# Performance work log

Hardware: AMD Instinct MI355X
Metric: run time of the kernel (lower is better)

Reference implementation:

```python
import jax, jax.numpy as jnp
import numpy as np

NUM_HEADS = 12
HEAD_DIM = 64
NPT = 1  # num_prefix_tokens

def _rot(x):
    # pairs (x0,x1) -> (-x1, x0), matching timm's rot()
    x2 = x.reshape(*x.shape[:-1], -1, 2)
    r = jnp.stack([-x2[..., 1], x2[..., 0]], axis=-1)
    return r.reshape(x.shape)

def _apply_rope_cat(x, rope):
    # rope: [N_rot, 2*hd] = sin||cos concatenated
    sin, cos = jnp.split(rope, 2, axis=-1)
    return x * cos + _rot(x) * sin

def setup_inputs() -> dict:
    key = jax.random.key(0)
    ks = jax.random.split(key, 7)
    B, N, C = 8, 4097, 768
    hd = HEAD_DIM
    x = jax.random.normal(ks[0], (B, N, C), jnp.float32)
    rope = jax.random.normal(ks[1], (N - NPT, 2 * hd), jnp.float32)
    qkv_w = jax.random.normal(ks[2], (3 * C, C), jnp.float32) * (C ** -0.5)
    q_bias = jax.random.normal(ks[3], (C,), jnp.float32) * 0.02
    v_bias = jax.random.normal(ks[4], (C,), jnp.float32) * 0.02
    proj_w = jax.random.normal(ks[5], (C, C), jnp.float32) * (C ** -0.5)
    proj_b = jax.random.normal(ks[6], (C,), jnp.float32) * 0.02
    return dict(x=x, rope=rope, qkv_w=qkv_w, q_bias=q_bias, v_bias=v_bias,
                proj_w=proj_w, proj_b=proj_b)

def reference(x, rope, qkv_w, q_bias, v_bias, proj_w, proj_b):
    B, N, C = x.shape
    H, hd = NUM_HEADS, HEAD_DIM
    # fused QKV with k_bias fixed at zero (non-trainable buffer)
    bias = jnp.concatenate([q_bias, jnp.zeros_like(q_bias), v_bias])
    qkv = x @ qkv_w.T + bias                            # [B,N,3C]
    qkv = qkv.reshape(B, N, 3, H, hd).transpose(2, 0, 3, 1, 4)
    q, k, v = qkv[0], qkv[1], qkv[2]                    # [B,H,N,hd]
    # RoPE on all tokens except the prefix (CLS) token
    q = jnp.concatenate([q[:, :, :NPT], _apply_rope_cat(q[:, :, NPT:], rope)], axis=2)
    k = jnp.concatenate([k[:, :, :NPT], _apply_rope_cat(k[:, :, NPT:], rope)], axis=2)
    # linear attention: kv = K^T V, then Q @ kv, normalized by hd*N
    kv = jnp.einsum('bhnd,bhne->bhde', k, v)            # [B,H,hd,hd]
    out = jnp.einsum('bhnd,bhde->bhne', q, kv) / hd / N # [B,H,N,hd]
    out = out.transpose(0, 2, 1, 3).reshape(B, N, C)
    return out @ proj_w.T + proj_b
```

## Files before the change

### kernel.cpp

```cpp
#include <hip/hip_runtime.h>
#include <hip/hip_bf16.h>

typedef __attribute__((ext_vector_type(8))) short short8;
typedef __attribute__((ext_vector_type(4))) float f32x4;

#define B_    8
#define N_    4097
#define C_    768
#define M_TOT (B_*N_)
#define K3    (3*C_)
#define CHUNKS 16
#define NSTEP 24

__device__ __forceinline__ float bf2f(unsigned short u) {
  union { unsigned int i; float f; } x; x.i = ((unsigned int)u) << 16; return x.f;
}
__device__ __forceinline__ unsigned short f2bf(float f) {
  union { float f; unsigned int i; } x; x.f = f;
  unsigned int i = x.i + 0x7fffu + ((x.i >> 16) & 1u);
  return (unsigned short)(i >> 16);
}
__device__ __forceinline__ void gload16(const void* g, void* l) {
  __builtin_amdgcn_global_load_lds(
      (const __attribute__((address_space(1))) void*)g,
      (__attribute__((address_space(3))) void*)l, 16, 0, 0);
}

__global__ __launch_bounds__(256) void cvt_kernel(const float* __restrict__ inx,
                                                  unsigned short* __restrict__ outx,
                                                  const float* __restrict__ inw,
                                                  unsigned short* __restrict__ outw,
                                                  long n4x, long n4tot) {
  long i = (long)blockIdx.x * blockDim.x + threadIdx.x;
  long stride = (long)gridDim.x * blockDim.x;
  for (; i < n4tot; i += stride) {
    const float4* src; ushort4* dst; long j;
    if (i < n4x) { src = (const float4*)inx; dst = (ushort4*)outx; j = i; }
    else         { src = (const float4*)inw; dst = (ushort4*)outw; j = i - n4x; }
    float4 v = src[j];
    ushort4 o;
    o.x = f2bf(v.x); o.y = f2bf(v.y); o.z = f2bf(v.z); o.w = f2bf(v.w);
    dst[j] = o;
  }
}

__global__ __launch_bounds__(512, 4) void gemm_qkv_rope(
    const unsigned short* __restrict__ A,
    const unsigned short* __restrict__ Bw,
    const float* __restrict__ rope,
    const float* __restrict__ qb,
    const float* __restrict__ vb,
    unsigned short* __restrict__ qkv)
{
  __shared__ __align__(16) char L[3*24576];
  const int tid  = threadIdx.x;
  const int wave = tid >> 6, lane = tid & 63;
  const int lr = lane & 15, lk = lane >> 4;
  const int wm = wave >> 2, wn = wave & 3;

  const int o = blockIdx.x;
  const int xcd = o & 7, loc = o >> 3;
  const int tile = (xcd < 1 ? xcd*290 : 290 + (xcd-1)*289) + loc;
  const int m0 = (tile / 9) * 128;
  const int n0 = (tile % 9) * 256;

  const int arow = tid >> 2, achk = tid & 3;
  const int am = min(m0 + arow, M_TOT-1);
  const unsigned short* gA  = A  + (long)am*768 + achk*8;
  const unsigned short* gB1 = Bw + (long)(n0 + arow)*768 + achk*8;
  const unsigned short* gB2 = Bw + (long)(n0 + arow + 128)*768 + achk*8;
  const int dA  = wave*1024;
  const int dB1 = 8192  + wave*1024;
  const int dB2 = 16384 + wave*1024;

  const int abase = (wm*64 + lr)*64 + lk*16;
  const int bbase = 8192 + (wn*64 + lr)*64 + lk*16;

  f32x4 acc[4][4];
#pragma unroll
  for (int i = 0; i < 4; ++i)
#pragma unroll
    for (int j = 0; j < 4; ++j) acc[i][j] = (f32x4){0.f,0.f,0.f,0.f};

  auto STAGE = [&](int buf, int kk) {
    char* sb = L + buf*24576;
    gload16(gA  + kk, sb + dA);
    gload16(gB1 + kk, sb + dB1);
    gload16(gB2 + kk, sb + dB2);
  };
  auto COMPUTE = [&](int buf) {
    const char* sb = L + buf*24576;
    short8 af[4], bfr[4];
#pragma unroll
    for (int mi = 0; mi < 4; ++mi)
      af[mi] = *(const short8*)(sb + abase + mi*1024);
#pragma unroll
    for (int ni = 0; ni < 4; ++ni)
      bfr[ni] = *(const short8*)(sb + bbase + ni*1024);
#pragma unroll
    for (int mi = 0; mi < 4; ++mi)
#pragma unroll
      for (int ni = 0; ni < 4; ++ni)
        acc[mi][ni] = __builtin_amdgcn_mfma_f32_16x16x32_bf16(af[mi], bfr[ni], acc[mi][ni], 0, 0, 0);
  };

  STAGE(0, 0);
  STAGE(1, 32);
  asm volatile("s_waitcnt vmcnt(3)" ::: "memory");
  __builtin_amdgcn_s_barrier();
  __builtin_amdgcn_sched_barrier(0);

  int cur = 0;
  for (int tt = 0; tt < NSTEP-2; ++tt) {
    int stg = cur + 2; if (stg >= 3) stg -= 3;
    STAGE(stg, (tt+2)*32);
    COMPUTE(cur);
    asm volatile("s_waitcnt vmcnt(3)" ::: "memory");
    __builtin_amdgcn_sched_barrier(0);
    __builtin_amdgcn_s_barrier();
    __builtin_amdgcn_sched_barrier(0);
    cur = (cur + 1 == 3) ? 0 : cur + 1;
  }
  COMPUTE(cur);
  asm volatile("s_waitcnt vmcnt(0)" ::: "memory");
  __builtin_amdgcn_sched_barrier(0);
  __builtin_amdgcn_s_barrier();
  __builtin_amdgcn_sched_barrier(0);
  cur = (cur + 1 == 3) ? 0 : cur + 1;
  COMPUTE(cur);

  const int which = n0 / 768;
  unsigned short* plane = qkv + (long)which*M_TOT*768;
#pragma unroll
  for (int mi = 0; mi < 4; ++mi) {
#pragma unroll
    for (int ni = 0; ni < 4; ++ni) {
      const int gc = n0 + wn*64 + ni*16 + lr;
      const int within = gc - which*768;
      const int d = within & 63;
      float bias = 0.f;
      if (which == 0) bias = qb[within];
      else if (which == 2) bias = vb[within];
#pragma unroll
      for (int r = 0; r < 4; ++r) {
        const int gm = m0 + wm*64 + mi*16 + lk*4 + r;
        float v = acc[mi][ni][r] + bias;
        float pair = __shfl_xor(v, 1);
        float vo = v;
        if (which < 2) {
          const int ntok = gm % 4097;
          if (ntok > 0 && gm < M_TOT) {
            const float* rp = rope + (long)(ntok - 1)*128 + d;
            const float s = rp[0], c = rp[64];
            const float rot = (d & 1) ? pair : -pair;
            vo = v*c + rot*s;
          }
        }
        if (gm < M_TOT) plane[(long)gm*768 + within] = f2bf(vo);
      }
    }
  }
}

__global__ __launch_bounds__(256) void kv_partial_kernel(
    const unsigned short* __restrict__ qkv, float* __restrict__ part)
{
  const int bh = blockIdx.y;
  const int b = bh / 12, h = bh % 12;
  const int chunk = blockIdx.x;
  const int per = (N_ + CHUNKS - 1) / CHUNKS;
  const int nst = chunk * per;
  const int nen = min(nst + per, N_);
  const unsigned short* Kpl = qkv + (long)M_TOT*768 + ((long)b*N_)*768 + h*64;
  const unsigned short* Vpl = qkv + (long)2*M_TOT*768 + ((long)b*N_)*768 + h*64;
  __shared__ unsigned short Kl[32*64];
  __shared__ unsigned short Vl[32*64];
  const int t = threadIdx.x;
  const int ty = t >> 4, tx = t & 15;
  const int lrow = t >> 3, lpc = t & 7;
  float acc[4][4] = {};
  for (int nb = nst; nb < nen; nb += 32) {
    const int cnt = min(32, nen - nb);
    __syncthreads();
    if (lrow < cnt) {
      *(uint4*)(Kl + lrow*64 + lpc*8) = *(const uint4*)(Kpl + (long)(nb + lrow)*768 + lpc*8);
      *(uint4*)(Vl + lrow*64 + lpc*8) = *(const uint4*)(Vpl + (long)(nb + lrow)*768 + lpc*8);
    }
    __syncthreads();
#pragma unroll 2
    for (int i = 0; i < cnt; ++i) {
      const ushort4 ku = *(const ushort4*)(Kl + i*64 + ty*4);
      const ushort4 vu = *(const ushort4*)(Vl + i*64 + tx*4);
      float kf[4] = {bf2f(ku.x), bf2f(ku.y), bf2f(ku.z), bf2f(ku.w)};
      float vf[4] = {bf2f(vu.x), bf2f(vu.y), bf2f(vu.z), bf2f(vu.w)};
#pragma unroll
      for (int a = 0; a < 4; ++a)
#pragma unroll
        for (int e = 0; e < 4; ++e) acc[a][e] += kf[a]*vf[e];
    }
  }
  float* dst = part + ((long)chunk*96 + bh)*4096 + (ty*4)*64 + tx*4;
#pragma unroll
  for (int a = 0; a < 4; ++a)
#pragma unroll
    for (int e = 0; e < 4; ++e) dst[a*64 + e] = acc[a][e];
}

__global__ __launch_bounds__(256) void mcomb_kernel(const float* __restrict__ part,
                                                    const float* __restrict__ pw,
                                                    unsigned short* __restrict__ McT) {
  const int blk = blockIdx.x;
  const int cs = blk & 1;
  const int h  = (blk >> 1) % 12;
  const int b  = blk / 24;
  const int bh = b*12 + h;
  __shared__ float kvs[64][65];
  const int t = threadIdx.x;
  const int d_own = t >> 2;
  const int eg = (t & 3) * 16;

  float4 a0 = {0,0,0,0}, a1 = {0,0,0,0}, a2 = {0,0,0,0}, a3 = {0,0,0,0};
  const float4* p4 = (const float4*)part;
#pragma unroll
  for (int ch = 0; ch < CHUNKS; ++ch) {
    const long base = ((long)ch*96 + bh)*1024 + d_own*16 + (t & 3)*4;
    float4 v0 = p4[base+0], v1 = p4[base+1], v2 = p4[base+2], v3 = p4[base+3];
    a0.x += v0.x; a0.y += v0.y; a0.z += v0.z; a0.w += v0.w;
    a1.x += v1.x; a1.y += v1.y; a1.z += v1.z; a1.w += v1.w;
    a2.x += v2.x; a2.y += v2.y; a2.z += v2.z; a2.w += v2.w;
    a3.x += v3.x; a3.y += v3.y; a3.z += v3.z; a3.w += v3.w;
  }
  kvs[eg+ 0][d_own] = a0.x; kvs[eg+ 1][d_own] = a0.y; kvs[eg+ 2][d_own] = a0.z; kvs[eg+ 3][d_own] = a0.w;
  kvs[eg+ 4][d_own] = a1.x; kvs[eg+ 5][d_own] = a1.y; kvs[eg+ 6][d_own] = a1.z; kvs[eg+ 7][d_own] = a1.w;
  kvs[eg+ 8][d_own] = a2.x; kvs[eg+ 9][d_own] = a2.y; kvs[eg+10][d_own] = a2.z; kvs[eg+11][d_own] = a2.w;
  kvs[eg+12][d_own] = a3.x; kvs[eg+13][d_own] = a3.y; kvs[eg+14][d_own] = a3.z; kvs[eg+15][d_own] = a3.w;
  __syncthreads();

  const int lane = t & 63;
  const int w    = t >> 6;
  float kvcol[64];
#pragma unroll
  for (int e = 0; e < 64; ++e) kvcol[e] = kvs[e][lane];

  const float scale = (float)(1.0/(64.0*4097.0));
  const int cbase = cs*384 + w*96;
  for (int i = 0; i < 96; ++i) {
    const int c = cbase + i;
    const float* pwrow = pw + (long)c*768 + h*64;
    float s = 0.f;
#pragma unroll
    for (int e = 0; e < 64; ++e) s += pwrow[e] * kvcol[e];
    McT[((long)b*768 + c)*768 + h*64 + lane] = f2bf(s * scale);
  }
}

__global__ __launch_bounds__(512, 4) void gemm_final(
    const unsigned short* __restrict__ qkv,
    const unsigned short* __restrict__ McT,
    const float* __restrict__ pb,
    float* __restrict__ out)
{
  __shared__ __align__(16) char L[3*24576];
  const int tid  = threadIdx.x;
  const int wave = tid >> 6, lane = tid & 63;
  const int lr = lane & 15, lk = lane >> 4;
  const int wm = wave >> 2, wn = wave & 3;

  const int o = blockIdx.x;
  const int xcd = o & 7, loc = o >> 3;
  const int b  = xcd;
  const int mt = loc / 3, ct = loc % 3;
  const int m0 = mt * 128;
  const int c0 = ct * 256;

  const int arow = tid >> 2, achk = tid & 3;
  const int am = min(m0 + arow, N_-1);
  const unsigned short* gA  = qkv + ((long)b*N_ + am)*768 + achk*8;
  const unsigned short* Bb  = McT + (long)b*768*768;
  const unsigned short* gB1 = Bb + (long)(c0 + arow)*768 + achk*8;
  const unsigned short* gB2 = Bb + (long)(c0 + arow + 128)*768 + achk*8;
  const int dA  = wave*1024;
  const int dB1 = 8192  + wave*1024;
  const int dB2 = 16384 + wave*1024;

  const int abase = (wm*64 + lr)*64 + lk*16;
  const int bbase = 8192 + (wn*64 + lr)*64 + lk*16;

  f32x4 acc[4][4];
#pragma unroll
  for (int i = 0; i < 4; ++i)
#pragma unroll
    for (int j = 0; j < 4; ++j) acc[i][j] = (f32x4){0.f,0.f,0.f,0.f};

  auto STAGE = [&](int buf, int kk) {
    char* sb = L + buf*24576;
    gload16(gA  + kk, sb + dA);
    gload16(gB1 + kk, sb + dB1);
    gload16(gB2 + kk, sb + dB2);
  };
  auto COMPUTE = [&](int buf) {
    const char* sb = L + buf*24576;
    short8 af[4], bfr[4];
#pragma unroll
    for (int mi = 0; mi < 4; ++mi)
      af[mi] = *(const short8*)(sb + abase + mi*1024);
#pragma unroll
    for (int ni = 0; ni < 4; ++ni)
      bfr[ni] = *(const short8*)(sb + bbase + ni*1024);
#pragma unroll
    for (int mi = 0; mi < 4; ++mi)
#pragma unroll
      for (int ni = 0; ni < 4; ++ni)
        acc[mi][ni] = __builtin_amdgcn_mfma_f32_16x16x32_bf16(af[mi], bfr[ni], acc[mi][ni], 0, 0, 0);
  };

  STAGE(0, 0);
  STAGE(1, 32);
  asm volatile("s_waitcnt vmcnt(3)" ::: "memory");
  __builtin_amdgcn_s_barrier();
  __builtin_amdgcn_sched_barrier(0);

  int cur = 0;
  for (int tt = 0; tt < NSTEP-2; ++tt) {
    int stg = cur + 2; if (stg >= 3) stg -= 3;
    STAGE(stg, (tt+2)*32);
    COMPUTE(cur);
    asm volatile("s_waitcnt vmcnt(3)" ::: "memory");
    __builtin_amdgcn_sched_barrier(0);
    __builtin_amdgcn_s_barrier();
    __builtin_amdgcn_sched_barrier(0);
    cur = (cur + 1 == 3) ? 0 : cur + 1;
  }
  COMPUTE(cur);
  asm volatile("s_waitcnt vmcnt(0)" ::: "memory");
  __builtin_amdgcn_sched_barrier(0);
  __builtin_amdgcn_s_barrier();
  __builtin_amdgcn_sched_barrier(0);
  cur = (cur + 1 == 3) ? 0 : cur + 1;
  COMPUTE(cur);

#pragma unroll
  for (int mi = 0; mi < 4; ++mi) {
#pragma unroll
    for (int ni = 0; ni < 4; ++ni) {
      const int gc = c0 + wn*64 + ni*16 + lr;
      const float bias = pb[gc];
#pragma unroll
      for (int r = 0; r < 4; ++r) {
        const int tok = m0 + wm*64 + mi*16 + lk*4 + r;
        if (tok < N_)
          out[((long)b*N_ + tok)*768 + gc] = acc[mi][ni][r] + bias;
      }
    }
  }
}

extern "C" void kernel_launch(void* const* d_in, const int* in_sizes, int n_in,
                              void* d_out, int out_size, void* d_ws, size_t ws_size,
                              hipStream_t stream) {
  const float* x      = (const float*)d_in[0];
  const float* rope   = (const float*)d_in[1];
  const float* qkv_w  = (const float*)d_in[2];
  const float* q_bias = (const float*)d_in[3];
  const float* v_bias = (const float*)d_in[4];
  const float* proj_w = (const float*)d_in[5];
  const float* proj_b = (const float*)d_in[6];
  float* out = (float*)d_out;

  char* w0 = (char*)d_ws;
  unsigned short* x_bf  = (unsigned short*)w0;
  unsigned short* wq_bf = (unsigned short*)(w0 + 50343936);
  unsigned short* qkv   = (unsigned short*)(w0 + 50343936 + 3538944);
  float*          part  = (float*)w0;
  unsigned short* McT   = (unsigned short*)(w0 + 25165824 + 1572864);

  const long n4x = (long)M_TOT*768/4;
  const long n4w = (long)K3*768/4;
  cvt_kernel<<<2048, 256, 0, stream>>>(x, x_bf, qkv_w, wq_bf, n4x, n4x + n4w);

  gemm_qkv_rope<<<2313, 512, 0, stream>>>(x_bf, wq_bf, rope, q_bias, v_bias, qkv);

  kv_partial_kernel<<<dim3(CHUNKS, 96), 256, 0, stream>>>(qkv, part);
  mcomb_kernel<<<192, 256, 0, stream>>>(part, proj_w, McT);

  gemm_final<<<792, 512, 0, stream>>>(qkv, McT, proj_b, out);
}
```

Baseline: 434.5 us.

## Use 4-wave blocks with 64x128 per-wave tiles in both GEMMs

Both bf16 GEMMs move from 8 waves per 128x256 block to 4 waves, so each wave computes a 64x128 sub-tile (4x8 MFMA accumulators) instead of 64x64. Each thread now issues six global-to-LDS loads per stage, and the waitcnt thresholds are adjusted to match. The larger per-wave tile raises MFMA work per LDS fragment load and halves the number of waves that must sync at each barrier. The cost is about twice the accumulator registers and fewer resident waves to hide latency.

```diff
diff --git a/kernel.cpp b/kernel.cpp
--- a/kernel.cpp
+++ b/kernel.cpp
@@ -44,7 +44,7 @@
   }
 }
 
-__global__ __launch_bounds__(512, 4) void gemm_qkv_rope(
+__global__ __launch_bounds__(256, 2) void gemm_qkv_rope(
     const unsigned short* __restrict__ A,
     const unsigned short* __restrict__ Bw,
     const float* __restrict__ rope,
@@ -56,7 +56,7 @@
   const int tid  = threadIdx.x;
   const int wave = tid >> 6, lane = tid & 63;
   const int lr = lane & 15, lk = lane >> 4;
-  const int wm = wave >> 2, wn = wave & 3;
+  const int wm = wave >> 1, wn = wave & 1;
 
   const int o = blockIdx.x;
   const int xcd = o & 7, loc = o >> 3;
@@ -64,49 +64,53 @@
   const int m0 = (tile / 9) * 128;
   const int n0 = (tile % 9) * 256;
 
-  const int arow = tid >> 2, achk = tid & 3;
-  const int am = min(m0 + arow, M_TOT-1);
-  const unsigned short* gA  = A  + (long)am*768 + achk*8;
-  const unsigned short* gB1 = Bw + (long)(n0 + arow)*768 + achk*8;
-  const unsigned short* gB2 = Bw + (long)(n0 + arow + 128)*768 + achk*8;
-  const int dA  = wave*1024;
-  const int dB1 = 8192  + wave*1024;
-  const int dB2 = 16384 + wave*1024;
+  const int srow = tid >> 2, schk = tid & 3;
+  const int amA0 = min(m0 + srow,      M_TOT-1);
+  const int amA1 = min(m0 + 64 + srow, M_TOT-1);
+  const unsigned short* gA0 = A + (long)amA0*768 + schk*8;
+  const unsigned short* gA1 = A + (long)amA1*768 + schk*8;
+  const unsigned short* gB0 = Bw + (long)(n0 +   0 + srow)*768 + schk*8;
+  const unsigned short* gB1 = Bw + (long)(n0 +  64 + srow)*768 + schk*8;
+  const unsigned short* gB2 = Bw + (long)(n0 + 128 + srow)*768 + schk*8;
+  const unsigned short* gB3 = Bw + (long)(n0 + 192 + srow)*768 + schk*8;
+  const int dT = tid*16;
 
   const int abase = (wm*64 + lr)*64 + lk*16;
-  const int bbase = 8192 + (wn*64 + lr)*64 + lk*16;
-
-  f32x4 acc[4][4];
+  const int bbase = 8192 + (wn*128 + lr)*64 + lk*16;
+
+  f32x4 acc[4][8];
 #pragma unroll
   for (int i = 0; i < 4; ++i)
 #pragma unroll
-    for (int j = 0; j < 4; ++j) acc[i][j] = (f32x4){0.f,0.f,0.f,0.f};
+    for (int j = 0; j < 8; ++j) acc[i][j] = (f32x4){0.f,0.f,0.f,0.f};
 
   auto STAGE = [&](int buf, int kk) {
     char* sb = L + buf*24576;
-    gload16(gA  + kk, sb + dA);
-    gload16(gB1 + kk, sb + dB1);
-    gload16(gB2 + kk, sb + dB2);
+    gload16(gA0 + kk, sb + dT);
+    gload16(gA1 + kk, sb + 4096 + dT);
+    gload16(gB0 + kk, sb + 8192 + dT);
+    gload16(gB1 + kk, sb + 12288 + dT);
+    gload16(gB2 + kk, sb + 16384 + dT);
+    gload16(gB3 + kk, sb + 20480 + dT);
   };
   auto COMPUTE = [&](int buf) {
     const char* sb = L + buf*24576;
-    short8 af[4], bfr[4];
-#pragma unroll
-    for (int mi = 0; mi < 4; ++mi)
-      af[mi] = *(const short8*)(sb + abase + mi*1024);
-#pragma unroll
-    for (int ni = 0; ni < 4; ++ni)
+    short8 bfr[8];
+#pragma unroll
+    for (int ni = 0; ni < 8; ++ni)
       bfr[ni] = *(const short8*)(sb + bbase + ni*1024);
 #pragma unroll
-    for (int mi = 0; mi < 4; ++mi)
-#pragma unroll
-      for (int ni = 0; ni < 4; ++ni)
-        acc[mi][ni] = __builtin_amdgcn_mfma_f32_16x16x32_bf16(af[mi], bfr[ni], acc[mi][ni], 0, 0, 0);
+    for (int mi = 0; mi < 4; ++mi) {
+      short8 af = *(const short8*)(sb + abase + mi*1024);
+#pragma unroll
+      for (int ni = 0; ni < 8; ++ni)
+        acc[mi][ni] = __builtin_amdgcn_mfma_f32_16x16x32_bf16(af, bfr[ni], acc[mi][ni], 0, 0, 0);
+    }
   };
 
   STAGE(0, 0);
   STAGE(1, 32);
-  asm volatile("s_waitcnt vmcnt(3)" ::: "memory");
+  asm volatile("s_waitcnt vmcnt(6)" ::: "memory");
   __builtin_amdgcn_s_barrier();
   __builtin_amdgcn_sched_barrier(0);
 
@@ -115,7 +119,7 @@
     int stg = cur + 2; if (stg >= 3) stg -= 3;
     STAGE(stg, (tt+2)*32);
     COMPUTE(cur);
-    asm volatile("s_waitcnt vmcnt(3)" ::: "memory");
+    asm volatile("s_waitcnt vmcnt(6)" ::: "memory");
     __builtin_amdgcn_sched_barrier(0);
     __builtin_amdgcn_s_barrier();
     __builtin_amdgcn_sched_barrier(0);
@@ -134,8 +138,8 @@
 #pragma unroll
   for (int mi = 0; mi < 4; ++mi) {
 #pragma unroll
-    for (int ni = 0; ni < 4; ++ni) {
-      const int gc = n0 + wn*64 + ni*16 + lr;
+    for (int ni = 0; ni < 8; ++ni) {
+      const int gc = n0 + wn*128 + ni*16 + lr;
       const int within = gc - which*768;
       const int d = within & 63;
       float bias = 0.f;
@@ -254,7 +258,7 @@
   }
 }
 
-__global__ __launch_bounds__(512, 4) void gemm_final(
+__global__ __launch_bounds__(256, 2) void gemm_final(
     const unsigned short* __restrict__ qkv,
     const unsigned short* __restrict__ McT,
     const float* __restrict__ pb,
@@ -264,7 +268,7 @@
   const int tid  = threadIdx.x;
   const int wave = tid >> 6, lane = tid & 63;
   const int lr = lane & 15, lk = lane >> 4;
-  const int wm = wave >> 2, wn = wave & 3;
+  const int wm = wave >> 1, wn = wave & 1;
 
   const int o = blockIdx.x;
   const int xcd = o & 7, loc = o >> 3;
@@ -273,50 +277,54 @@
   const int m0 = mt * 128;
   const int c0 = ct * 256;
 
-  const int arow = tid >> 2, achk = tid & 3;
-  const int am = min(m0 + arow, N_-1);
-  const unsigned short* gA  = qkv + ((long)b*N_ + am)*768 + achk*8;
+  const int srow = tid >> 2, schk = tid & 3;
+  const int amA0 = min(m0 + srow,      N_-1);
+  const int amA1 = min(m0 + 64 + srow, N_-1);
+  const unsigned short* gA0 = qkv + ((long)b*N_ + amA0)*768 + schk*8;
+  const unsigned short* gA1 = qkv + ((long)b*N_ + amA1)*768 + schk*8;
   const unsigned short* Bb  = McT + (long)b*768*768;
-  const unsigned short* gB1 = Bb + (long)(c0 + arow)*768 + achk*8;
-  const unsigned short* gB2 = Bb + (long)(c0 + arow + 128)*768 + achk*8;
-  const int dA  = wave*1024;
-  const int dB1 = 8192  + wave*1024;
-  const int dB2 = 16384 + wave*1024;
+  const unsigned short* gB0 = Bb + (long)(c0 +   0 + srow)*768 + schk*8;
+  const unsigned short* gB1 = Bb + (long)(c0 +  64 + srow)*768 + schk*8;
+  const unsigned short* gB2 = Bb + (long)(c0 + 128 + srow)*768 + schk*8;
+  const unsigned short* gB3 = Bb + (long)(c0 + 192 + srow)*768 + schk*8;
+  const int dT = tid*16;
 
   const int abase = (wm*64 + lr)*64 + lk*16;
-  const int bbase = 8192 + (wn*64 + lr)*64 + lk*16;
-
-  f32x4 acc[4][4];
+  const int bbase = 8192 + (wn*128 + lr)*64 + lk*16;
+
+  f32x4 acc[4][8];
 #pragma unroll
   for (int i = 0; i < 4; ++i)
 #pragma unroll
-    for (int j = 0; j < 4; ++j) acc[i][j] = (f32x4){0.f,0.f,0.f,0.f};
+    for (int j = 0; j < 8; ++j) acc[i][j] = (f32x4){0.f,0.f,0.f,0.f};
 
   auto STAGE = [&](int buf, int kk) {
     char* sb = L + buf*24576;
-    gload16(gA  + kk, sb + dA);
-    gload16(gB1 + kk, sb + dB1);
-    gload16(gB2 + kk, sb + dB2);
+    gload16(gA0 + kk, sb + dT);
+    gload16(gA1 + kk, sb + 4096 + dT);
+    gload16(gB0 + kk, sb + 8192 + dT);
+    gload16(gB1 + kk, sb + 12288 + dT);
+    gload16(gB2 + kk, sb + 16384 + dT);
+    gload16(gB3 + kk, sb + 20480 + dT);
   };
   auto COMPUTE = [&](int buf) {
     const char* sb = L + buf*24576;
-    short8 af[4], bfr[4];
-#pragma unroll
-    for (int mi = 0; mi < 4; ++mi)
-      af[mi] = *(const short8*)(sb + abase + mi*1024);
-#pragma unroll
-    for (int ni = 0; ni < 4; ++ni)
+    short8 bfr[8];
+#pragma unroll
+    for (int ni = 0; ni < 8; ++ni)
       bfr[ni] = *(const short8*)(sb + bbase + ni*1024);
 #pragma unroll
-    for (int mi = 0; mi < 4; ++mi)
-#pragma unroll
-      for (int ni = 0; ni < 4; ++ni)
-        acc[mi][ni] = __builtin_amdgcn_mfma_f32_16x16x32_bf16(af[mi], bfr[ni], acc[mi][ni], 0, 0, 0);
+    for (int mi = 0; mi < 4; ++mi) {
+      short8 af = *(const short8*)(sb + abase + mi*1024);
+#pragma unroll
+      for (int ni = 0; ni < 8; ++ni)
+        acc[mi][ni] = __builtin_amdgcn_mfma_f32_16x16x32_bf16(af, bfr[ni], acc[mi][ni], 0, 0, 0);
+    }
   };
 
   STAGE(0, 0);
   STAGE(1, 32);
-  asm volatile("s_waitcnt vmcnt(3)" ::: "memory");
+  asm volatile("s_waitcnt vmcnt(6)" ::: "memory");
   __builtin_amdgcn_s_barrier();
   __builtin_amdgcn_sched_barrier(0);
 
@@ -325,7 +333,7 @@
     int stg = cur + 2; if (stg >= 3) stg -= 3;
     STAGE(stg, (tt+2)*32);
     COMPUTE(cur);
-    asm volatile("s_waitcnt vmcnt(3)" ::: "memory");
+    asm volatile("s_waitcnt vmcnt(6)" ::: "memory");
     __builtin_amdgcn_sched_barrier(0);
     __builtin_amdgcn_s_barrier();
     __builtin_amdgcn_sched_barrier(0);
@@ -342,8 +350,8 @@
 #pragma unroll
   for (int mi = 0; mi < 4; ++mi) {
 #pragma unroll
-    for (int ni = 0; ni < 4; ++ni) {
-      const int gc = c0 + wn*64 + ni*16 + lr;
+    for (int ni = 0; ni < 8; ++ni) {
+      const int gc = c0 + wn*128 + ni*16 + lr;
       const float bias = pb[gc];
 #pragma unroll
       for (int r = 0; r < 4; ++r) {
@@ -378,10 +386,10 @@
   const long n4w = (long)K3*768/4;
   cvt_kernel<<<2048, 256, 0, stream>>>(x, x_bf, qkv_w, wq_bf, n4x, n4x + n4w);
 
-  gemm_qkv_rope<<<2313, 512, 0, stream>>>(x_bf, wq_bf, rope, q_bias, v_bias, qkv);
+  gemm_qkv_rope<<<2313, 256, 0, stream>>>(x_bf, wq_bf, rope, q_bias, v_bias, qkv);
 
   kv_partial_kernel<<<dim3(CHUNKS, 96), 256, 0, stream>>>(qkv, part);
   mcomb_kernel<<<192, 256, 0, stream>>>(part, proj_w, McT);
 
-  gemm_final<<<792, 512, 0, stream>>>(qkv, McT, proj_b, out);
-}
+  gemm_final<<<792, 256, 0, stream>>>(qkv, McT, proj_b, out);
+}
```

After: 483.2 us. 11.2% more time.
